# Performance work log

Hardware: AMD Instinct MI355X
Metric: run time of the kernel (lower is better)

## Reference

```python
import jax, jax.numpy as jnp
import numpy as np

D_MODEL = 1024
D_STATE = 16
D_CONV = 4
EXPAND = 2
D_INNER = EXPAND * D_MODEL  # 2048
DT_RANK = 16  # per source: list(range(1,17))[-1] since d_inner >= 16
BATCH = 2
SEQ = 1024


def setup_inputs() -> dict:
    key = jax.random.key(0)
    ks = jax.random.split(key, 8)
    s = 0.02
    return {
        "x": jax.random.normal(ks[0], (BATCH, SEQ, D_MODEL), jnp.float32),
        # torch Linear convention: weight [out, in]
        "in_proj_w": jax.random.normal(ks[1], (2 * D_INNER, D_MODEL), jnp.float32) * s,
        "in_proj_b": jnp.zeros((2 * D_INNER,), jnp.float32),
        # depthwise conv: [d_inner, 1, d_conv]
        "conv_w": jax.random.normal(ks[2], (D_INNER, 1, D_CONV), jnp.float32) * s,
        "conv_b": jnp.zeros((D_INNER,), jnp.float32),
        "x_proj_w": jax.random.normal(ks[3], (DT_RANK + 2 * D_STATE, D_INNER), jnp.float32) * s,
        "x_proj_b": jnp.zeros((DT_RANK + 2 * D_STATE,), jnp.float32),
        "dt_proj_w": jax.random.normal(ks[4], (D_INNER, DT_RANK), jnp.float32) * s,
        "dt_proj_b": jnp.zeros((D_INNER,), jnp.float32),
        "A_log": jnp.log(jnp.broadcast_to(jnp.arange(1, D_STATE + 1, dtype=jnp.float32), (D_INNER, D_STATE))),
        "D": jnp.ones((D_INNER,), jnp.float32),
        "out_proj_w": jax.random.normal(ks[5], (D_MODEL, D_INNER), jnp.float32) * s,
        "out_proj_b": jnp.zeros((D_MODEL,), jnp.float32),
    }


def _mamba(x, in_proj_w, in_proj_b, conv_w, conv_b, x_proj_w, x_proj_b,
           dt_proj_w, dt_proj_b, A_log, D, out_proj_w, out_proj_b):
    # in_proj and split into x / res branches
    x_and_res = x @ in_proj_w.T + in_proj_b                       # [B, L, 2*d_inner]
    xs, res = jnp.split(x_and_res, [D_INNER], axis=-1)
    # causal depthwise conv: left-pad d_conv-1, which matches padding=d_conv-1 then [:, :, :l]
    xc = jnp.transpose(xs, (0, 2, 1))                             # [B, d_inner, L]
    xc = jax.lax.conv_general_dilated(
        xc, conv_w, window_strides=(1,), padding=[(D_CONV - 1, 0)],
        feature_group_count=D_INNER, dimension_numbers=("NCH", "OIH", "NCH"))
    xc = xc + conv_b[None, :, None]
    xs = jax.nn.silu(jnp.transpose(xc, (0, 2, 1)))                # [B, L, d_inner]

    # SSM input-dependent parameters
    x_dbl = xs @ x_proj_w.T + x_proj_b                            # [B, L, dt_rank + 2n]
    dlt, Bm, Cm = jnp.split(x_dbl, [DT_RANK, DT_RANK + D_STATE], axis=-1)
    delta = jax.nn.softplus(dlt @ dt_proj_w.T + dt_proj_b)        # [B, L, d_inner]
    A = -jnp.exp(A_log)                                           # [d_inner, n]

    # selective scan over time
    def step(h, inputs):
        d_t, x_t, b_t, c_t = inputs                               # [B,d],[B,d],[B,n],[B,n]
        dA = jnp.exp(d_t[:, :, None] * A)                         # [B, d, n]
        h = dA * h + (d_t * x_t)[:, :, None] * b_t[:, None, :]    # [B, d, n]
        y_t = jnp.einsum("bdn,bn->bd", h, c_t)                   # [B, d]
        return h, y_t

    h0 = jnp.zeros((xs.shape[0], D_INNER, D_STATE), xs.dtype)
    seq_inputs = (jnp.moveaxis(delta, 1, 0), jnp.moveaxis(xs, 1, 0),
                  jnp.moveaxis(Bm, 1, 0), jnp.moveaxis(Cm, 1, 0))
    _, ys = jax.lax.scan(step, h0, seq_inputs)                    # ys: [L, B, d_inner]
    y = jnp.moveaxis(ys, 0, 1) + xs * D                           # skip term D

    y = y * jax.nn.silu(res)                                      # gating
    return y @ out_proj_w.T + out_proj_b                          # [B, L, d_model]


def reference(x, in_proj_w, in_proj_b, conv_w, conv_b, x_proj_w, x_proj_b,
              dt_proj_w, dt_proj_b, A_log, D, out_proj_w, out_proj_b):
    return _mamba(x, in_proj_w, in_proj_b, conv_w, conv_b, x_proj_w, x_proj_b,
                  dt_proj_w, dt_proj_b, A_log, D, out_proj_w, out_proj_b)
```

## Files before the change

### kernel.cpp

```cpp
#include <hip/hip_runtime.h>

#define D_MODEL 1024
#define D_STATE 16
#define D_CONV  4
#define D_INNER 2048
#define DT_RANK 16
#define BATCH   2
#define SEQ     1024
#define M_ROWS  (BATCH*SEQ)
#define CHUNK   32
#define NCHUNK  (SEQ/CHUNK)

typedef __bf16 bf16x8 __attribute__((ext_vector_type(8)));
typedef float  f32x4  __attribute__((ext_vector_type(4)));

__device__ __forceinline__ unsigned short f2bf(float f) {
  unsigned u = __float_as_uint(f);
  u += 0x7fffu + ((u >> 16) & 1u);
  return (unsigned short)(u >> 16);
}

__device__ __forceinline__ float sigmoid_fast(float v) {
  return 1.f / (1.f + __expf(-v));
}

__device__ __forceinline__ float softplus_f(float s) {
  return (s > 20.f) ? s : __logf(1.f + __expf(s));
}

__global__ __launch_bounds__(256) void cast_all_kernel(
    const float* __restrict__ x, const float* __restrict__ w1, const float* __restrict__ w2,
    const float* __restrict__ xpw,
    unsigned short* __restrict__ xbf, unsigned short* __restrict__ w1bf,
    unsigned short* __restrict__ w2bf, unsigned short* __restrict__ xpwbf) {
  const int N0 = (M_ROWS * D_MODEL) / 4;
  const int N1 = (2 * D_INNER * D_MODEL) / 4;
  const int N2 = (D_MODEL * D_INNER) / 4;
  int i = blockIdx.x * 256 + threadIdx.x;
  const float* src; unsigned short* dst; int off;
  if (i < N0)                 { src = x;   dst = xbf;   off = i; }
  else if (i < N0 + N1)       { src = w1;  dst = w1bf;  off = i - N0; }
  else if (i < N0 + N1 + N2)  { src = w2;  dst = w2bf;  off = i - N0 - N1; }
  else                        { src = xpw; dst = xpwbf; off = i - N0 - N1 - N2; }
  float4 v = *(const float4*)(src + (size_t)off * 4);
  ushort4 o;
  o.x = f2bf(v.x); o.y = f2bf(v.y); o.z = f2bf(v.z); o.w = f2bf(v.w);
  *(ushort4*)(dst + (size_t)off * 4) = o;
}

__global__ __launch_bounds__(256) void gemm_bf16_nt(
    const __bf16* __restrict__ A, const __bf16* __restrict__ B,
    const float* __restrict__ bias, float* __restrict__ C,
    int M, int N, int K) {
  __shared__ __bf16 As[128][40];
  __shared__ __bf16 Bs[128][40];
  const int tid  = threadIdx.x;
  const int lane = tid & 63;
  const int w    = tid >> 6;
  const int wr   = w >> 1, wc = w & 1;
  const int rowBase = blockIdx.y * 128;
  const int colBase = blockIdx.x * 128;

  f32x4 acc[4][4];
  #pragma unroll
  for (int i = 0; i < 4; ++i)
    #pragma unroll
    for (int j = 0; j < 4; ++j) {
      f32x4 z = {0.f, 0.f, 0.f, 0.f};
      acc[i][j] = z;
    }

  const int sr = tid >> 2;
  const int ss = (tid & 3) * 8;
  const int fr = lane & 15;
  const int fk = (lane >> 4) * 8;

  for (int k0 = 0; k0 < K; k0 += 32) {
    const __bf16* Ap = A + (size_t)(rowBase + sr) * K + k0 + ss;
    const __bf16* Bp = B + (size_t)(colBase + sr) * K + k0 + ss;
    *(bf16x8*)&As[sr][ss]      = *(const bf16x8*)Ap;
    *(bf16x8*)&As[sr + 64][ss] = *(const bf16x8*)(Ap + (size_t)64 * K);
    *(bf16x8*)&Bs[sr][ss]      = *(const bf16x8*)Bp;
    *(bf16x8*)&Bs[sr + 64][ss] = *(const bf16x8*)(Bp + (size_t)64 * K);
    __syncthreads();

    bf16x8 af[4], bfr[4];
    #pragma unroll
    for (int mm = 0; mm < 4; ++mm)
      af[mm] = *(const bf16x8*)&As[wr * 64 + mm * 16 + fr][fk];
    #pragma unroll
    for (int nn = 0; nn < 4; ++nn)
      bfr[nn] = *(const bf16x8*)&Bs[wc * 64 + nn * 16 + fr][fk];
    #pragma unroll
    for (int mm = 0; mm < 4; ++mm)
      #pragma unroll
      for (int nn = 0; nn < 4; ++nn)
        acc[mm][nn] = __builtin_amdgcn_mfma_f32_16x16x32_bf16(af[mm], bfr[nn], acc[mm][nn], 0, 0, 0);
    __syncthreads();
  }

  #pragma unroll
  for (int nn = 0; nn < 4; ++nn) {
    int col = colBase + wc * 64 + nn * 16 + (lane & 15);
    float bv = bias[col];
    #pragma unroll
    for (int mm = 0; mm < 4; ++mm) {
      int row0 = rowBase + wr * 64 + mm * 16 + (lane >> 4) * 4;
      #pragma unroll
      for (int r = 0; r < 4; ++r)
        C[(size_t)(row0 + r) * N + col] = acc[mm][nn][r] + bv;
    }
  }
}

__global__ __launch_bounds__(256) void conv_silu_kernel(
    const float* __restrict__ xar, const float* __restrict__ cw,
    const float* __restrict__ cb, float* __restrict__ xs,
    unsigned short* __restrict__ xsbf) {
  int idx = blockIdx.x * 256 + threadIdx.x;
  int m  = idx >> 9;
  int d4 = (idx & 511) << 2;
  int t  = m & (SEQ - 1);
  float a0 = 0.f, a1 = 0.f, a2 = 0.f, a3 = 0.f;
  #pragma unroll
  for (int j = 0; j < 4; ++j) {
    int tt = t - 3 + j;
    if (tt < 0) continue;
    const float4 v = *(const float4*)&xar[(size_t)(m - 3 + j) * (2 * D_INNER) + d4];
    a0 += v.x * cw[(d4 + 0) * 4 + j];
    a1 += v.y * cw[(d4 + 1) * 4 + j];
    a2 += v.z * cw[(d4 + 2) * 4 + j];
    a3 += v.w * cw[(d4 + 3) * 4 + j];
  }
  a0 += cb[d4 + 0]; a1 += cb[d4 + 1]; a2 += cb[d4 + 2]; a3 += cb[d4 + 3];
  float4 o;
  o.x = a0 * sigmoid_fast(a0);
  o.y = a1 * sigmoid_fast(a1);
  o.z = a2 * sigmoid_fast(a2);
  o.w = a3 * sigmoid_fast(a3);
  *(float4*)&xs[(size_t)m * D_INNER + d4] = o;
  ushort4 ob;
  ob.x = f2bf(o.x); ob.y = f2bf(o.y); ob.z = f2bf(o.z); ob.w = f2bf(o.w);
  *(ushort4*)&xsbf[(size_t)m * D_INNER + d4] = ob;
}

__global__ __launch_bounds__(256) void xproj_mfma(
    const __bf16* __restrict__ A, const __bf16* __restrict__ B,
    const float* __restrict__ xpb,
    float* __restrict__ dlt, float* __restrict__ Bm, float* __restrict__ Cm) {
  __shared__ __bf16 As[128][40];
  __shared__ __bf16 Bs[48][40];
  const int tid  = threadIdx.x;
  const int lane = tid & 63;
  const int w    = tid >> 6;
  const int rowBase = blockIdx.x * 128;

  f32x4 acc[2][3];
  #pragma unroll
  for (int i = 0; i < 2; ++i)
    #pragma unroll
    for (int j = 0; j < 3; ++j) {
      f32x4 z = {0.f, 0.f, 0.f, 0.f};
      acc[i][j] = z;
    }

  const int sr = tid >> 2;
  const int ss = (tid & 3) * 8;
  const int fr = lane & 15;
  const int fk = (lane >> 4) * 8;

  for (int k0 = 0; k0 < D_INNER; k0 += 32) {
    const __bf16* Ap = A + (size_t)(rowBase + sr) * D_INNER + k0 + ss;
    *(bf16x8*)&As[sr][ss]      = *(const bf16x8*)Ap;
    *(bf16x8*)&As[sr + 64][ss] = *(const bf16x8*)(Ap + (size_t)64 * D_INNER);
    if (tid < 192)
      *(bf16x8*)&Bs[tid >> 2][ss] = *(const bf16x8*)(B + (size_t)(tid >> 2) * D_INNER + k0 + ss);
    __syncthreads();

    bf16x8 af[2], bfr[3];
    #pragma unroll
    for (int mm = 0; mm < 2; ++mm)
      af[mm] = *(const bf16x8*)&As[w * 32 + mm * 16 + fr][fk];
    #pragma unroll
    for (int nn = 0; nn < 3; ++nn)
      bfr[nn] = *(const bf16x8*)&Bs[nn * 16 + fr][fk];
    #pragma unroll
    for (int mm = 0; mm < 2; ++mm)
      #pragma unroll
      for (int nn = 0; nn < 3; ++nn)
        acc[mm][nn] = __builtin_amdgcn_mfma_f32_16x16x32_bf16(af[mm], bfr[nn], acc[mm][nn], 0, 0, 0);
    __syncthreads();
  }

  const int c16 = lane & 15;
  #pragma unroll
  for (int nn = 0; nn < 3; ++nn) {
    float bv = xpb[nn * 16 + c16];
    float* dst = (nn == 0) ? dlt : (nn == 1) ? Bm : Cm;
    #pragma unroll
    for (int mm = 0; mm < 2; ++mm) {
      int row0 = rowBase + w * 32 + mm * 16 + (lane >> 4) * 4;
      #pragma unroll
      for (int r = 0; r < 4; ++r)
        dst[(size_t)(row0 + r) * 16 + c16] = acc[mm][nn][r] + bv;
    }
  }
}


#define DELTA16(sarr, ttq)                                                       \
  {                                                                              \
    float4 q0 = *(const float4*)&sarr[ttq][0];                                   \
    float4 q1 = *(const float4*)&sarr[ttq][4];                                   \
    float4 q2 = *(const float4*)&sarr[ttq][8];                                   \
    float4 q3 = *(const float4*)&sarr[ttq][12];                                  \
    s += q0.x*dtwr[0] + q0.y*dtwr[1] + q0.z*dtwr[2] + q0.w*dtwr[3];              \
    s += q1.x*dtwr[4] + q1.y*dtwr[5] + q1.z*dtwr[6] + q1.w*dtwr[7];              \
    s += q2.x*dtwr[8] + q2.y*dtwr[9] + q2.z*dtwr[10] + q2.w*dtwr[11];            \
    s += q3.x*dtwr[12] + q3.y*dtwr[13] + q3.z*dtwr[14] + q3.w*dtwr[15];          \
  }

__global__ __launch_bounds__(256) void scan_phase1(
    const float* __restrict__ xs, const float* __restrict__ dlt,
    const float* __restrict__ Bmat, const float* __restrict__ dtw,
    const float* __restrict__ dtb, const float* __restrict__ alog,
    float* __restrict__ Hbuf, float* __restrict__ Sbuf) {
  __shared__ float dltS[CHUNK][16];
  __shared__ float BS[CHUNK][16];
  const int tid = threadIdx.x;
  const int c   = blockIdx.y;
  const int b   = blockIdx.z;
  const int d   = blockIdx.x * 256 + tid;
  const int row0 = b * SEQ + c * CHUNK;
  {
    int e = tid * 2;
    int tt = e >> 4, r = e & 15;
    *(float2*)&dltS[tt][r] = *(const float2*)&dlt[(row0 + tt) * 16 + r];
    *(float2*)&BS[tt][r]   = *(const float2*)&Bmat[(row0 + tt) * 16 + r];
  }
  float dtwr[16], An[16];
  #pragma unroll
  for (int q = 0; q < 4; ++q) {
    float4 w4 = *(const float4*)&dtw[d * 16 + q * 4];
    dtwr[q*4+0] = w4.x; dtwr[q*4+1] = w4.y; dtwr[q*4+2] = w4.z; dtwr[q*4+3] = w4.w;
    float4 a4 = *(const float4*)&alog[d * 16 + q * 4];
    An[q*4+0] = -__expf(a4.x); An[q*4+1] = -__expf(a4.y);
    An[q*4+2] = -__expf(a4.z); An[q*4+3] = -__expf(a4.w);
  }
  const float dtbv = dtb[d];
  float xv[CHUNK];
  #pragma unroll
  for (int tt = 0; tt < CHUNK; ++tt)
    xv[tt] = xs[(size_t)(row0 + tt) * D_INNER + d];
  __syncthreads();
  float dv[CHUNK];
  #pragma unroll
  for (int tt = 0; tt < CHUNK; ++tt) {
    float s = dtbv;
    DELTA16(dltS, tt);
    dv[tt] = softplus_f(s);
  }
  float h[16];
  #pragma unroll
  for (int n = 0; n < 16; ++n) h[n] = 0.f;
  float Ssum = 0.f;
  #pragma unroll
  for (int tt = 0; tt < CHUNK; ++tt) {
    const float dvt = dv[tt];
    Ssum += dvt;
    const float dvx = dvt * xv[tt];
    float4 B0 = *(const float4*)&BS[tt][0];
    float4 B1 = *(const float4*)&BS[tt][4];
    float4 B2 = *(const float4*)&BS[tt][8];
    float4 B3 = *(const float4*)&BS[tt][12];
    h[0]  = __expf(dvt*An[0])*h[0]   + dvx*B0.x;
    h[1]  = __expf(dvt*An[1])*h[1]   + dvx*B0.y;
    h[2]  = __expf(dvt*An[2])*h[2]   + dvx*B0.z;
    h[3]  = __expf(dvt*An[3])*h[3]   + dvx*B0.w;
    h[4]  = __expf(dvt*An[4])*h[4]   + dvx*B1.x;
    h[5]  = __expf(dvt*An[5])*h[5]   + dvx*B1.y;
    h[6]  = __expf(dvt*An[6])*h[6]   + dvx*B1.z;
    h[7]  = __expf(dvt*An[7])*h[7]   + dvx*B1.w;
    h[8]  = __expf(dvt*An[8])*h[8]   + dvx*B2.x;
    h[9]  = __expf(dvt*An[9])*h[9]   + dvx*B2.y;
    h[10] = __expf(dvt*An[10])*h[10] + dvx*B2.z;
    h[11] = __expf(dvt*An[11])*h[11] + dvx*B2.w;
    h[12] = __expf(dvt*An[12])*h[12] + dvx*B3.x;
    h[13] = __expf(dvt*An[13])*h[13] + dvx*B3.y;
    h[14] = __expf(dvt*An[14])*h[14] + dvx*B3.z;
    h[15] = __expf(dvt*An[15])*h[15] + dvx*B3.w;
  }
  size_t hbase = (((size_t)(b * NCHUNK + c) * D_INNER) + d) * 16;
  #pragma unroll
  for (int q = 0; q < 4; ++q) {
    float4 o = {h[q*4+0], h[q*4+1], h[q*4+2], h[q*4+3]};
    *(float4*)&Hbuf[hbase + q*4] = o;
  }
  Sbuf[((size_t)b * NCHUNK + c) * D_INNER + d] = Ssum;
}

__global__ __launch_bounds__(256) void scan_phase2(
    const float* __restrict__ alog, const float* __restrict__ Sbuf,
    float* __restrict__ Hbuf) {
  const int tid = threadIdx.x;
  const int n  = tid & 15;
  const int dl = tid >> 4;
  const int d  = blockIdx.x * 16 + dl;
  const int b  = blockIdx.y;
  const float An = -__expf(alog[d * 16 + n]);
  float h_run = 0.f;
  #pragma unroll 4
  for (int c = 0; c < NCHUNK; ++c) {
    size_t idx = (((size_t)(b * NCHUNK + c) * D_INNER) + d) * 16 + n;
    float hend = Hbuf[idx];
    float P = __expf(An * Sbuf[((size_t)b * NCHUNK + c) * D_INNER + d]);
    Hbuf[idx] = h_run;
    h_run = P * h_run + hend;
  }
}

__global__ __launch_bounds__(256) void scan_phase3(
    const float* __restrict__ xs, const float* __restrict__ xar,
    const float* __restrict__ dlt, const float* __restrict__ Bmat,
    const float* __restrict__ Cmat, const float* __restrict__ dtw,
    const float* __restrict__ dtb, const float* __restrict__ alog,
    const float* __restrict__ Dvec, const float* __restrict__ Hbuf,
    unsigned short* __restrict__ ybf) {
  __shared__ float dltS[CHUNK][16];
  __shared__ float BS[CHUNK][16];
  __shared__ float CS[CHUNK][16];
  const int tid = threadIdx.x;
  const int c   = blockIdx.y;
  const int b   = blockIdx.z;
  const int d   = blockIdx.x * 256 + tid;
  const int row0 = b * SEQ + c * CHUNK;
  {
    int e = tid * 2;
    int tt = e >> 4, r = e & 15;
    *(float2*)&dltS[tt][r] = *(const float2*)&dlt[(row0 + tt) * 16 + r];
    *(float2*)&BS[tt][r]   = *(const float2*)&Bmat[(row0 + tt) * 16 + r];
    *(float2*)&CS[tt][r]   = *(const float2*)&Cmat[(row0 + tt) * 16 + r];
  }
  float dtwr[16], An[16];
  #pragma unroll
  for (int q = 0; q < 4; ++q) {
    float4 w4 = *(const float4*)&dtw[d * 16 + q * 4];
    dtwr[q*4+0] = w4.x; dtwr[q*4+1] = w4.y; dtwr[q*4+2] = w4.z; dtwr[q*4+3] = w4.w;
    float4 a4 = *(const float4*)&alog[d * 16 + q * 4];
    An[q*4+0] = -__expf(a4.x); An[q*4+1] = -__expf(a4.y);
    An[q*4+2] = -__expf(a4.z); An[q*4+3] = -__expf(a4.w);
  }
  const float dtbv = dtb[d];
  const float Dn   = Dvec[d];
  float h[16];
  {
    size_t hbase = (((size_t)(b * NCHUNK + c) * D_INNER) + d) * 16;
    #pragma unroll
    for (int q = 0; q < 4; ++q) {
      float4 hv = *(const float4*)&Hbuf[hbase + q*4];
      h[q*4+0] = hv.x; h[q*4+1] = hv.y; h[q*4+2] = hv.z; h[q*4+3] = hv.w;
    }
  }
  float xv[CHUNK], rv[CHUNK];
  #pragma unroll
  for (int tt = 0; tt < CHUNK; ++tt) {
    xv[tt] = xs[(size_t)(row0 + tt) * D_INNER + d];
    rv[tt] = xar[(size_t)(row0 + tt) * (2 * D_INNER) + D_INNER + d];
  }
  __syncthreads();
  float dv[CHUNK];
  #pragma unroll
  for (int tt = 0; tt < CHUNK; ++tt) {
    float s = dtbv;
    DELTA16(dltS, tt);
    dv[tt] = softplus_f(s);
  }
  #pragma unroll
  for (int tt = 0; tt < CHUNK; ++tt) {
    const float dvt = dv[tt];
    const float dvx = dvt * xv[tt];
    float4 B0 = *(const float4*)&BS[tt][0];
    float4 B1 = *(const float4*)&BS[tt][4];
    float4 B2 = *(const float4*)&BS[tt][8];
    float4 B3 = *(const float4*)&BS[tt][12];
    float4 C0 = *(const float4*)&CS[tt][0];
    float4 C1 = *(const float4*)&CS[tt][4];
    float4 C2 = *(const float4*)&CS[tt][8];
    float4 C3 = *(const float4*)&CS[tt][12];
    float y = 0.f;
    h[0]  = __expf(dvt*An[0])*h[0]   + dvx*B0.x;  y += h[0]*C0.x;
    h[1]  = __expf(dvt*An[1])*h[1]   + dvx*B0.y;  y += h[1]*C0.y;
    h[2]  = __expf(dvt*An[2])*h[2]   + dvx*B0.z;  y += h[2]*C0.z;
    h[3]  = __expf(dvt*An[3])*h[3]   + dvx*B0.w;  y += h[3]*C0.w;
    h[4]  = __expf(dvt*An[4])*h[4]   + dvx*B1.x;  y += h[4]*C1.x;
    h[5]  = __expf(dvt*An[5])*h[5]   + dvx*B1.y;  y += h[5]*C1.y;
    h[6]  = __expf(dvt*An[6])*h[6]   + dvx*B1.z;  y += h[6]*C1.z;
    h[7]  = __expf(dvt*An[7])*h[7]   + dvx*B1.w;  y += h[7]*C1.w;
    h[8]  = __expf(dvt*An[8])*h[8]   + dvx*B2.x;  y += h[8]*C2.x;
    h[9]  = __expf(dvt*An[9])*h[9]   + dvx*B2.y;  y += h[9]*C2.y;
    h[10] = __expf(dvt*An[10])*h[10] + dvx*B2.z;  y += h[10]*C2.z;
    h[11] = __expf(dvt*An[11])*h[11] + dvx*B2.w;  y += h[11]*C2.w;
    h[12] = __expf(dvt*An[12])*h[12] + dvx*B3.x;  y += h[12]*C3.x;
    h[13] = __expf(dvt*An[13])*h[13] + dvx*B3.y;  y += h[13]*C3.y;
    h[14] = __expf(dvt*An[14])*h[14] + dvx*B3.z;  y += h[14]*C3.z;
    h[15] = __expf(dvt*An[15])*h[15] + dvx*B3.w;  y += h[15]*C3.w;
    y += xv[tt] * Dn;
    const float r = rv[tt];
    const float v = y * (r * sigmoid_fast(r));
    ybf[(size_t)(row0 + tt) * D_INNER + d] = f2bf(v);
  }
}

extern "C" void kernel_launch(void* const* d_in, const int* in_sizes, int n_in,
                              void* d_out, int out_size, void* d_ws, size_t ws_size,
                              hipStream_t stream) {
  const float* x    = (const float*)d_in[0];
  const float* ipw  = (const float*)d_in[1];
  const float* ipb  = (const float*)d_in[2];
  const float* cw   = (const float*)d_in[3];
  const float* cb   = (const float*)d_in[4];
  const float* xpw  = (const float*)d_in[5];
  const float* xpb  = (const float*)d_in[6];
  const float* dtw  = (const float*)d_in[7];
  const float* dtb  = (const float*)d_in[8];
  const float* alog = (const float*)d_in[9];
  const float* Dv   = (const float*)d_in[10];
  const float* opw  = (const float*)d_in[11];
  const float* opb  = (const float*)d_in[12];
  float* out = (float*)d_out;

  char* ws = (char*)d_ws;
  size_t off = 0;
  auto alloc = [&](size_t bytes) {
    char* p = ws + off;
    off += (bytes + 255) & ~(size_t)255;
    return p;
  };
  unsigned short* xbf   = (unsigned short*)alloc((size_t)M_ROWS * D_MODEL * 2);
  unsigned short* w1bf  = (unsigned short*)alloc((size_t)2 * D_INNER * D_MODEL * 2);
  unsigned short* w2bf  = (unsigned short*)alloc((size_t)D_MODEL * D_INNER * 2);
  unsigned short* xpwbf = (unsigned short*)alloc((size_t)48 * D_INNER * 2);
  float* xar = (float*)alloc((size_t)M_ROWS * 2 * D_INNER * 4);
  float* xsb = (float*)alloc((size_t)M_ROWS * D_INNER * 4);
  float* dlt = (float*)alloc((size_t)M_ROWS * 16 * 4);
  float* Bm  = (float*)alloc((size_t)M_ROWS * 16 * 4);
  float* Cm  = (float*)alloc((size_t)M_ROWS * 16 * 4);
  unsigned short* ybf = (unsigned short*)alloc((size_t)M_ROWS * D_INNER * 2);
  if (off > ws_size) return;
  unsigned short* xsbf = w1bf;
  float* Hbuf = (float*)w1bf;
  float* Sbuf = (float*)xbf;

  cast_all_kernel<<<8288, 256, 0, stream>>>(x, ipw, opw, xpw, xbf, w1bf, w2bf, xpwbf);
  gemm_bf16_nt<<<dim3(4096 / 128, 2048 / 128), 256, 0, stream>>>(
      (const __bf16*)xbf, (const __bf16*)w1bf, ipb, xar, M_ROWS, 2 * D_INNER, D_MODEL);
  conv_silu_kernel<<<4096, 256, 0, stream>>>(xar, cw, cb, xsb, xsbf);
  xproj_mfma<<<M_ROWS / 128, 256, 0, stream>>>(
      (const __bf16*)xsbf, (const __bf16*)xpwbf, xpb, dlt, Bm, Cm);
  scan_phase1<<<dim3(D_INNER / 256, NCHUNK, BATCH), 256, 0, stream>>>(
      xsb, dlt, Bm, dtw, dtb, alog, Hbuf, Sbuf);
  scan_phase2<<<dim3(D_INNER / 16, BATCH), 256, 0, stream>>>(alog, Sbuf, Hbuf);
  scan_phase3<<<dim3(D_INNER / 256, NCHUNK, BATCH), 256, 0, stream>>>(
      xsb, xar, dlt, Bm, Cm, dtw, dtb, alog, Dv, Hbuf, ybf);
  gemm_bf16_nt<<<dim3(1024 / 128, 2048 / 128), 256, 0, stream>>>(
      (const __bf16*)ybf, (const __bf16*)w2bf, opb, out, M_ROWS, D_MODEL, D_INNER);
}
```

Baseline: 306.7 us.

## Use direct global-to-LDS loads in GEMMs and shrink out-proj tile rows

Both bf16 GEMMs now load A and B tiles with global_load_lds 16-byte transfers straight into shared memory, skipping the trip through registers. The shared-memory padding is removed to fit the contiguous layout those loads need, which can cause bank conflicts on the fragment reads. The kernel is templated on tile rows, and the output projection uses 64-row tiles so it launches twice as many blocks and fills more CUs. There is still no double buffering.

```diff
diff --git a/kernel.cpp b/kernel.cpp
--- a/kernel.cpp
+++ b/kernel.cpp
@@ -26,6 +26,12 @@
 
 __device__ __forceinline__ float softplus_f(float s) {
   return (s > 20.f) ? s : __logf(1.f + __expf(s));
+}
+
+__device__ __forceinline__ void gll16(const void* g, void* l) {
+  __builtin_amdgcn_global_load_lds(
+      (const __attribute__((address_space(1))) unsigned int*)g,
+      (__attribute__((address_space(3))) unsigned int*)l, 16, 0, 0);
 }
 
 __global__ __launch_bounds__(256) void cast_all_kernel(
@@ -48,51 +54,54 @@
   *(ushort4*)(dst + (size_t)off * 4) = o;
 }
 
-__global__ __launch_bounds__(256) void gemm_bf16_nt(
+template<int BM>
+__global__ __launch_bounds__(256) void gemm_gll(
     const __bf16* __restrict__ A, const __bf16* __restrict__ B,
     const float* __restrict__ bias, float* __restrict__ C,
     int M, int N, int K) {
-  __shared__ __bf16 As[128][40];
-  __shared__ __bf16 Bs[128][40];
+  constexpr int MR = BM / 32;
+  __shared__ __bf16 As[BM][32];
+  __shared__ __bf16 Bs[128][32];
   const int tid  = threadIdx.x;
   const int lane = tid & 63;
   const int w    = tid >> 6;
   const int wr   = w >> 1, wc = w & 1;
-  const int rowBase = blockIdx.y * 128;
+  const int rowBase = blockIdx.y * BM;
   const int colBase = blockIdx.x * 128;
 
-  f32x4 acc[4][4];
-  #pragma unroll
-  for (int i = 0; i < 4; ++i)
-    #pragma unroll
-    for (int j = 0; j < 4; ++j) {
-      f32x4 z = {0.f, 0.f, 0.f, 0.f};
-      acc[i][j] = z;
-    }
-
-  const int sr = tid >> 2;
-  const int ss = (tid & 3) * 8;
-  const int fr = lane & 15;
-  const int fk = (lane >> 4) * 8;
+  f32x4 acc[MR][4];
+  #pragma unroll
+  for (int i = 0; i < MR; ++i)
+    #pragma unroll
+    for (int j = 0; j < 4; ++j) { f32x4 z = {0.f,0.f,0.f,0.f}; acc[i][j] = z; }
+
+  const int srow = lane >> 2;
+  const int sk   = (lane & 3) * 8;
+  const int fr   = lane & 15;
+  const int fk   = (lane >> 4) * 8;
 
   for (int k0 = 0; k0 < K; k0 += 32) {
-    const __bf16* Ap = A + (size_t)(rowBase + sr) * K + k0 + ss;
-    const __bf16* Bp = B + (size_t)(colBase + sr) * K + k0 + ss;
-    *(bf16x8*)&As[sr][ss]      = *(const bf16x8*)Ap;
-    *(bf16x8*)&As[sr + 64][ss] = *(const bf16x8*)(Ap + (size_t)64 * K);
-    *(bf16x8*)&Bs[sr][ss]      = *(const bf16x8*)Bp;
-    *(bf16x8*)&Bs[sr + 64][ss] = *(const bf16x8*)(Bp + (size_t)64 * K);
+    #pragma unroll
+    for (int i = 0; i < BM / 64; ++i) {
+      const int r0 = w * (BM / 4) + i * 16;
+      gll16(A + (size_t)(rowBase + r0 + srow) * K + k0 + sk, &As[r0][0]);
+    }
+    #pragma unroll
+    for (int i = 0; i < 2; ++i) {
+      const int r0 = w * 32 + i * 16;
+      gll16(B + (size_t)(colBase + r0 + srow) * K + k0 + sk, &Bs[r0][0]);
+    }
     __syncthreads();
 
-    bf16x8 af[4], bfr[4];
-    #pragma unroll
-    for (int mm = 0; mm < 4; ++mm)
-      af[mm] = *(const bf16x8*)&As[wr * 64 + mm * 16 + fr][fk];
+    bf16x8 af[MR], bfr[4];
+    #pragma unroll
+    for (int mm = 0; mm < MR; ++mm)
+      af[mm] = *(const bf16x8*)&As[wr * (BM / 2) + mm * 16 + fr][fk];
     #pragma unroll
     for (int nn = 0; nn < 4; ++nn)
       bfr[nn] = *(const bf16x8*)&Bs[wc * 64 + nn * 16 + fr][fk];
     #pragma unroll
-    for (int mm = 0; mm < 4; ++mm)
+    for (int mm = 0; mm < MR; ++mm)
       #pragma unroll
       for (int nn = 0; nn < 4; ++nn)
         acc[mm][nn] = __builtin_amdgcn_mfma_f32_16x16x32_bf16(af[mm], bfr[nn], acc[mm][nn], 0, 0, 0);
@@ -101,11 +110,11 @@
 
   #pragma unroll
   for (int nn = 0; nn < 4; ++nn) {
-    int col = colBase + wc * 64 + nn * 16 + (lane & 15);
+    int col = colBase + wc * 64 + nn * 16 + fr;
     float bv = bias[col];
     #pragma unroll
-    for (int mm = 0; mm < 4; ++mm) {
-      int row0 = rowBase + wr * 64 + mm * 16 + (lane >> 4) * 4;
+    for (int mm = 0; mm < MR; ++mm) {
+      int row0 = rowBase + wr * (BM / 2) + mm * 16 + (lane >> 4) * 4;
       #pragma unroll
       for (int r = 0; r < 4; ++r)
         C[(size_t)(row0 + r) * N + col] = acc[mm][nn][r] + bv;
@@ -452,7 +461,7 @@
   float* Sbuf = (float*)xbf;
 
   cast_all_kernel<<<8288, 256, 0, stream>>>(x, ipw, opw, xpw, xbf, w1bf, w2bf, xpwbf);
-  gemm_bf16_nt<<<dim3(4096 / 128, 2048 / 128), 256, 0, stream>>>(
+  gemm_gll<128><<<dim3(4096 / 128, 2048 / 128), 256, 0, stream>>>(
       (const __bf16*)xbf, (const __bf16*)w1bf, ipb, xar, M_ROWS, 2 * D_INNER, D_MODEL);
   conv_silu_kernel<<<4096, 256, 0, stream>>>(xar, cw, cb, xsb, xsbf);
   xproj_mfma<<<M_ROWS / 128, 256, 0, stream>>>(
@@ -462,6 +471,6 @@
   scan_phase2<<<dim3(D_INNER / 16, BATCH), 256, 0, stream>>>(alog, Sbuf, Hbuf);
   scan_phase3<<<dim3(D_INNER / 256, NCHUNK, BATCH), 256, 0, stream>>>(
       xsb, xar, dlt, Bm, Cm, dtw, dtb, alog, Dv, Hbuf, ybf);
-  gemm_bf16_nt<<<dim3(1024 / 128, 2048 / 128), 256, 0, stream>>>(
+  gemm_gll<64><<<dim3(1024 / 128, 2048 / 64), 256, 0, stream>>>(
       (const __bf16*)ybf, (const __bf16*)w2bf, opb, out, M_ROWS, D_MODEL, D_INNER);
 }
```

Result: faster. 297.3 us (-3.1%).
